# Kernel optimization log

Hardware: AMD Instinct MI355X
Metric: run time of the kernel (lower is better)

The kernel has to match this reference:

```python
import jax, jax.numpy as jnp
import numpy as np

N, E, C, NE, G, T = 20000, 320000, 32, 10, 64, 1000
NB, HID, LAYERS = 8, 64, 2
R_MAX, P_CUT, AVG_NEIGH = 5.0, 6, 16.0
LM = 16  # (max_ell+1)^2 spherical-harmonic components
L_OF_LM = jnp.array([0,1,1,1,2,2,2,2,2,3,3,3,3,3,3,3])


def sph_harm(u):
    # component-normalized real spherical harmonics up to l=3 on unit vectors u [E,3]
    x, y, z = u[:, 0], u[:, 1], u[:, 2]
    s3, s15, s5, s105, s7 = 3**0.5, 15**0.5, 5**0.5, 105**0.5, 7**0.5
    s35_8, s21_8 = (35.0/8.0)**0.5, (21.0/8.0)**0.5
    comps = [jnp.ones_like(x),
             s3*x, s3*y, s3*z,
             s15*x*y, s15*y*z, 0.5*s5*(3*z*z-1.0), s15*x*z, 0.5*s15*(x*x-y*y),
             s35_8*y*(3*x*x-y*y), s105*x*y*z, s21_8*y*(5*z*z-1.0),
             0.5*s7*(5*z*z*z-3*z), s21_8*x*(5*z*z-1.0),
             0.5*s105*z*(x*x-y*y), s35_8*x*(x*x-3*y*y)]
    return jnp.stack(comps, axis=-1)  # [E,16]


def radial_embed(r):
    # Bessel basis with polynomial cutoff (MACE RadialEmbeddingBlock)
    n = jnp.arange(1, NB + 1, dtype=r.dtype)
    rc = jnp.maximum(r, 1e-9)
    bessel = (2.0/R_MAX)**0.5 * jnp.sin(n[None, :]*jnp.pi*rc[:, None]/R_MAX) / rc[:, None]
    xr = r / R_MAX
    p = float(P_CUT)
    f = (1.0 - 0.5*(p+1)*(p+2)*xr**p + p*(p+2)*xr**(p+1) - 0.5*p*(p+1)*xr**(p+2))
    f = f * (xr < 1.0)
    return bessel * f[:, None]  # [E,NB]


def setup_inputs():
    key = jax.random.key(0)
    ks = jax.random.split(key, 16)
    positions = jax.random.normal(ks[0], (N, 3)) * 3.0
    species = jax.random.randint(ks[1], (N,), 0, NE)
    node_attrs = jax.nn.one_hot(species, NE, dtype=jnp.float32)
    edge_index = jax.random.randint(ks[2], (2, E), 0, N)
    shifts = jnp.zeros((E, 3), jnp.float32)
    batch = jnp.sort(jax.random.randint(ks[3], (N,), 0, G))
    t = jax.random.randint(ks[4], (G,), 0, T)
    eps = jax.random.normal(ks[5], (N, NE + 3))
    betas = jnp.linspace(1e-4, 0.02, T)
    alpha_bar = jnp.cumprod(1.0 - betas)
    sc = 0.1
    W_embed = sc * jax.random.normal(ks[6], (NE + 1, C))
    W_r1 = sc * jax.random.normal(ks[7], (LAYERS, NB, HID))
    W_r2 = sc * jax.random.normal(ks[8], (LAYERS, HID, C * 4))
    W_mix = sc * jax.random.normal(ks[9], (LAYERS, 4, C, C))
    W_sc = sc * jax.random.normal(ks[10], (NE, C))
    W_prod = sc * jax.random.normal(ks[11], (LAYERS, 3, C))
    W_ro_s = sc * jax.random.normal(ks[12], (LAYERS, C, NE))
    W_ro_v = sc * jax.random.normal(ks[13], (LAYERS, C))
    return {"positions": positions, "node_attrs": node_attrs, "shifts": shifts,
            "eps": eps, "alpha_bar": alpha_bar, "W_embed": W_embed, "W_r1": W_r1,
            "W_r2": W_r2, "W_mix": W_mix, "W_sc": W_sc, "W_prod": W_prod,
            "W_ro_s": W_ro_s, "W_ro_v": W_ro_v, "edge_index": edge_index,
            "batch": batch, "t": t}


def reference(positions, node_attrs, shifts, eps, alpha_bar, W_embed, W_r1, W_r2,
              W_mix, W_sc, W_prod, W_ro_s, W_ro_v, edge_index, batch, t):
    sender, receiver = edge_index[0], edge_index[1]
    # diffusion: noise positions and attrs (DDPM q(x_t|x_0))
    ab = alpha_bar[t][batch][:, None]                       # [N,1]
    attrs0 = node_attrs / 4.0
    pos_noisy = jnp.sqrt(ab) * positions + jnp.sqrt(1.0 - ab) * eps[:, -3:]
    attrs_noisy = jnp.sqrt(ab) * attrs0 + jnp.sqrt(1.0 - ab) * eps[:, :NE]
    tf = (t.astype(jnp.float32) / T)[batch][:, None]
    h = jnp.concatenate([attrs_noisy, tf], axis=-1) @ W_embed  # [N,C]
    # edge geometry
    vec = pos_noisy[receiver] - pos_noisy[sender] + shifts
    r = jnp.sqrt(jnp.sum(vec * vec, axis=-1) + 1e-12)
    Y = sph_harm(vec / r[:, None])                          # [E,16]
    ef = radial_embed(r)                                    # [E,NB]
    scalar = h
    pred = jnp.zeros((N, NE + 3), h.dtype)
    for layer in range(LAYERS):
        rw = jax.nn.silu(ef @ W_r1[layer]) @ W_r2[layer]    # [E,4C]
        rw = rw.reshape(E, C, 4)[:, :, L_OF_LM]             # [E,C,16]
        msg = rw * scalar[sender][:, :, None] * Y[:, None, :]
        agg = jax.ops.segment_sum(msg, receiver, num_segments=N) / AVG_NEIGH
        Wm = W_mix[layer][L_OF_LM]                          # [16,C,C]
        feats = jnp.einsum('nck,kcd->ndk', agg, Wm)         # per-l channel mix
        s = feats[:, :, 0]
        poly = W_prod[layer, 0] + W_prod[layer, 1] * s + W_prod[layer, 2] * s * s
        feats = feats * poly[:, :, None]                    # correlation-3 product
        if layer == 0:
            feats = feats.at[:, :, 0].add(attrs_noisy @ W_sc)  # element skip
        scalar = feats[:, :, 0]
        pred_s = scalar @ W_ro_s[layer]                     # [N,NE]
        pred_v = jnp.einsum('ncm,c->nm', feats[:, :, 1:4], W_ro_v[layer])  # [N,3]
        pred = pred + jnp.concatenate([pred_s, pred_v], axis=-1)
    err = (pred - eps) ** 2
    loss_pos = jax.ops.segment_sum(err[:, -3:].sum(-1), batch, num_segments=G)
    loss_lab = jax.ops.segment_sum(err[:, :NE].sum(-1), batch, num_segments=G)
    nn = jax.ops.segment_sum(jnp.ones((N,), pred.dtype), batch, num_segments=G)
    loss = 0.5 * (loss_pos + loss_lab) / (jnp.maximum(nn, 1.0) * (3 + NE))
    return loss
```

## Files before the change

kernel.cpp:

```cpp
#include <hip/hip_runtime.h>

typedef unsigned short ushort_t;
typedef unsigned int uint_t;

#define NN 20000
#define EE 320000
#define CC 32
#define NEL 10
#define GG 64
#define TTT 1000
#define NBB 8
#define HIDD 64
#define EPB 256

typedef __attribute__((ext_vector_type(8))) short bf16x8;
typedef __attribute__((ext_vector_type(4))) float f32x4;

__device__ __forceinline__ float bits2f(uint_t b) { union { uint_t u; float f; } v; v.u = b; return v.f; }
__device__ __forceinline__ ushort_t f2b(float f) {
  union { float f; uint_t u; } v; v.f = f;
  uint_t r = (v.u + 0x7fffu + ((v.u >> 16) & 1u)) >> 16;
  return (ushort_t)r;
}
__device__ __forceinline__ uint_t pk(float a, float b) {
  return (uint_t)f2b(a) | ((uint_t)f2b(b) << 16);
}
__device__ __forceinline__ float lo16(uint_t u) { return bits2f(u << 16); }
__device__ __forceinline__ float hi16(uint_t u) { return bits2f(u & 0xffff0000u); }

__global__ __launch_bounds__(256) void k_prep(
    const float* __restrict__ positions, const float* __restrict__ node_attrs,
    const float* __restrict__ eps, const float* __restrict__ alpha_bar,
    const float* __restrict__ W_embed, const float* __restrict__ W_sc,
    const int* __restrict__ batch, const int* __restrict__ tarr,
    float* __restrict__ pos_noisy, float* __restrict__ scalA,
    float* __restrict__ sc_skip, float* __restrict__ pred, int* __restrict__ deg)
{
  int n = blockIdx.x * 256 + threadIdx.x;
  if (n >= NN) return;
  deg[n] = 0;
  int g = batch[n];
  int tn = tarr[g];
  float ab = alpha_bar[tn];
  float sa = sqrtf(ab), sb = sqrtf(fmaxf(1.0f - ab, 0.0f));
#pragma unroll
  for (int j = 0; j < 3; ++j)
    pos_noisy[n * 3 + j] = sa * positions[n * 3 + j] + sb * eps[n * 13 + 10 + j];
  float an[10];
#pragma unroll
  for (int j = 0; j < 10; ++j)
    an[j] = sa * 0.25f * node_attrs[n * 10 + j] + sb * eps[n * 13 + j];
  float tf = (float)tn * (1.0f / (float)TTT);
  for (int d = 0; d < CC; ++d) {
    float h = tf * W_embed[10 * CC + d];
    float sk = 0.0f;
#pragma unroll
    for (int j = 0; j < 10; ++j) {
      h = fmaf(an[j], W_embed[j * CC + d], h);
      sk = fmaf(an[j], W_sc[j * CC + d], sk);
    }
    scalA[n * CC + d] = h;
    sc_skip[n * CC + d] = sk;
  }
#pragma unroll
  for (int j = 0; j < 13; ++j) pred[n * 13 + j] = 0.0f;
}

__global__ __launch_bounds__(256) void k_edge_deg(const int* __restrict__ ei,
    int* __restrict__ deg)
{
  int e = blockIdx.x * 256 + threadIdx.x;
  atomicAdd(&deg[ei[EE + e]], 1);
}

__global__ __launch_bounds__(1024) void k_scan(const int* __restrict__ deg,
    int* __restrict__ offs, int* __restrict__ cursor,
    float* __restrict__ lnum, float* __restrict__ lcnt)
{
  __shared__ int wsums[16];
  __shared__ int woffs[16];
  int tid = threadIdx.x, lane = tid & 63, wv = tid >> 6;
  if (tid < GG) { lnum[tid] = 0.0f; lcnt[tid] = 0.0f; }
  int base = tid * 20;
  int loc[20];
  int s = 0;
#pragma unroll
  for (int j = 0; j < 20; ++j) {
    int idx = base + j;
    int v = (idx < NN) ? deg[idx] : 0;
    loc[j] = s; s += v;
  }
  int inc = s;
  for (int o = 1; o < 64; o <<= 1) {
    int v = __shfl_up(inc, o, 64);
    if (lane >= o) inc += v;
  }
  if (lane == 63) wsums[wv] = inc;
  __syncthreads();
  if (wv == 0 && lane < 16) {
    int v = wsums[lane];
    int i2 = v;
    for (int o = 1; o < 16; o <<= 1) {
      int vv = __shfl_up(i2, o, 16);
      if (lane >= o) i2 += vv;
    }
    woffs[lane] = i2 - v;
  }
  __syncthreads();
  int texcl = woffs[wv] + (inc - s);
#pragma unroll
  for (int j = 0; j < 20; ++j) {
    int idx = base + j;
    if (idx < NN) { int v = texcl + loc[j]; offs[idx] = v; cursor[idx] = v; }
  }
  if (tid == 1023) offs[NN] = EE;
}

__global__ __launch_bounds__(256) void k_edge2(
    const float* __restrict__ pos_noisy, const float* __restrict__ shifts,
    const int* __restrict__ ei, int* __restrict__ cursor,
    ushort_t* __restrict__ Ys, ushort_t* __restrict__ efs, int* __restrict__ snds)
{
  int e = blockIdx.x * 256 + threadIdx.x;
  int snd = ei[e], rcv = ei[EE + e];
  float vx = pos_noisy[rcv * 3 + 0] - pos_noisy[snd * 3 + 0] + shifts[e * 3 + 0];
  float vy = pos_noisy[rcv * 3 + 1] - pos_noisy[snd * 3 + 1] + shifts[e * 3 + 1];
  float vz = pos_noisy[rcv * 3 + 2] - pos_noisy[snd * 3 + 2] + shifts[e * 3 + 2];
  float r2 = vx * vx + vy * vy + vz * vz + 1e-12f;
  float r = sqrtf(r2);
  float inv = 1.0f / r;
  float x = vx * inv, y = vy * inv, z = vz * inv;

  const float s3 = 1.7320508075688772f, s15 = 3.872983346207417f, s5 = 2.23606797749979f;
  const float s105 = 10.246950765959598f, s7 = 2.6457513110645907f;
  const float s35_8 = 2.091650066335189f, s21_8 = 1.6201851746019651f;
  float yv[16];
  yv[0] = 1.0f;
  yv[1] = s3 * x; yv[2] = s3 * y; yv[3] = s3 * z;
  yv[4] = s15 * x * y;
  yv[5] = s15 * y * z;
  yv[6] = 0.5f * s5 * (3.0f * z * z - 1.0f);
  yv[7] = s15 * x * z;
  yv[8] = 0.5f * s15 * (x * x - y * y);
  yv[9] = s35_8 * y * (3.0f * x * x - y * y);
  yv[10] = s105 * x * y * z;
  yv[11] = s21_8 * y * (5.0f * z * z - 1.0f);
  yv[12] = 0.5f * s7 * (5.0f * z * z * z - 3.0f * z);
  yv[13] = s21_8 * x * (5.0f * z * z - 1.0f);
  yv[14] = 0.5f * s105 * z * (x * x - y * y);
  yv[15] = s35_8 * x * (x * x - 3.0f * y * y);

  float rc = fmaxf(r, 1e-9f);
  float pref = 0.6324555320336759f / rc;
  float th = 0.6283185307179586f * rc;
  float s1 = __sinf(th), c1 = __cosf(th);
  float xr = r * 0.2f;
  float fcut = 0.0f;
  if (xr < 1.0f) {
    float x2 = xr * xr, x3 = x2 * xr;
    float x6 = x3 * x3, x7 = x6 * xr, x8 = x7 * xr;
    fcut = 1.0f - 28.0f * x6 + 48.0f * x7 - 21.0f * x8;
  }
  float efv[8];
  float sp = 0.0f, scur = s1, c2 = 2.0f * c1;
#pragma unroll
  for (int b = 0; b < 8; ++b) {
    efv[b] = pref * scur * fcut;
    float nx = c2 * scur - sp;
    sp = scur; scur = nx;
  }

  int slot = atomicAdd(&cursor[rcv], 1);
  snds[slot] = snd;
  uint4* Y4 = (uint4*)Ys;
  Y4[(size_t)slot * 2 + 0] = make_uint4(pk(yv[0], yv[1]), pk(yv[2], yv[3]),
                                        pk(yv[4], yv[5]), pk(yv[6], yv[7]));
  Y4[(size_t)slot * 2 + 1] = make_uint4(pk(yv[8], yv[9]), pk(yv[10], yv[11]),
                                        pk(yv[12], yv[13]), pk(yv[14], yv[15]));
  ((uint4*)efs)[slot] = make_uint4(pk(efv[0], efv[1]), pk(efv[2], efv[3]),
                                   pk(efv[4], efv[5]), pk(efv[6], efv[7]));
}

__global__ __launch_bounds__(256) void k_rw_mfma(
    const ushort_t* __restrict__ efs, const float* __restrict__ W_r1,
    const float* __restrict__ W_r2, const int* __restrict__ snds,
    const float* __restrict__ scal_in, ushort_t* __restrict__ rwc, int layer)
{
  __shared__ __align__(16) ushort_t w2t[128][72];
  __shared__ __align__(16) ushort_t h1[EPB][72];
  int tid = threadIdx.x;
  const float* W1g = W_r1 + layer * NBB * HIDD;
  const float* W2g = W_r2 + layer * HIDD * 128;
  for (int idx = tid; idx < HIDD * 128; idx += 256) {
    int k = idx >> 7, n = idx & 127;
    w2t[n][k] = f2b(W2g[idx]);
  }
  {
    int e = blockIdx.x * EPB + tid;
    uint4 q = ((const uint4*)efs)[e];
    float efr[8] = {lo16(q.x), hi16(q.x), lo16(q.y), hi16(q.y),
                    lo16(q.z), hi16(q.z), lo16(q.w), hi16(q.w)};
    for (int hc = 0; hc < 8; ++hc) {
      float v[8];
#pragma unroll
      for (int hh = 0; hh < 8; ++hh) {
        int h = hc * 8 + hh;
        float t = 0.0f;
#pragma unroll
        for (int b = 0; b < 8; ++b) t = fmaf(efr[b], W1g[b * HIDD + h], t);
        v[hh] = t / (1.0f + __expf(-t));
      }
      *(uint4*)&h1[tid][hc * 8] = make_uint4(pk(v[0], v[1]), pk(v[2], v[3]),
                                             pk(v[4], v[5]), pk(v[6], v[7]));
    }
  }
  __syncthreads();
  int w = tid >> 6, lane = tid & 63;
  int c = lane & 15, quad = lane >> 4;
  bf16x8 bfr[16];
#pragma unroll
  for (int nt = 0; nt < 8; ++nt)
#pragma unroll
    for (int kt = 0; kt < 2; ++kt)
      bfr[nt * 2 + kt] = *(const bf16x8*)&w2t[nt * 16 + c][kt * 32 + quad * 8];
  int mb0 = w * 64;
#pragma unroll
  for (int mt = 0; mt < 4; ++mt) {
    int mbase = mb0 + mt * 16;
    bf16x8 a0 = *(const bf16x8*)&h1[mbase + c][quad * 8];
    bf16x8 a1 = *(const bf16x8*)&h1[mbase + c][32 + quad * 8];
    size_t erow = (size_t)blockIdx.x * EPB + mbase + quad * 4;
    int4 sn = *(const int4*)&snds[erow];
    const float* sb0 = scal_in + (size_t)sn.x * CC;
    const float* sb1 = scal_in + (size_t)sn.y * CC;
    const float* sb2 = scal_in + (size_t)sn.z * CC;
    const float* sb3 = scal_in + (size_t)sn.w * CC;
#pragma unroll
    for (int nt = 0; nt < 8; ++nt) {
      f32x4 acc = {0.0f, 0.0f, 0.0f, 0.0f};
      acc = __builtin_amdgcn_mfma_f32_16x16x32_bf16(a0, bfr[nt * 2 + 0], acc, 0, 0, 0);
      acc = __builtin_amdgcn_mfma_f32_16x16x32_bf16(a1, bfr[nt * 2 + 1], acc, 0, 0, 0);
      int col = nt * 16 + c;
      int cc = col >> 2;
      rwc[(erow + 0) * 128 + col] = f2b(acc[0] * sb0[cc]);
      rwc[(erow + 1) * 128 + col] = f2b(acc[1] * sb1[cc]);
      rwc[(erow + 2) * 128 + col] = f2b(acc[2] * sb2[cc]);
      rwc[(erow + 3) * 128 + col] = f2b(acc[3] * sb3[cc]);
    }
  }
}

__global__ __launch_bounds__(256) void k_layer(
    const ushort_t* __restrict__ Ys, const ushort_t* __restrict__ rwc,
    float* __restrict__ scal_out,
    const int* __restrict__ offs,
    const float* __restrict__ W_mix, const float* __restrict__ W_prod,
    const float* __restrict__ W_ro_s, const float* __restrict__ W_ro_v,
    const float* __restrict__ sc_skip, float* __restrict__ pred, int layer)
{
  __shared__ float lagg[4][CC][16];
  __shared__ float lf[4][CC][4];
  int w = threadIdx.x >> 6, lane = threadIdx.x & 63;
  int n = blockIdx.x * 4 + w;
  int c = lane >> 1;
  int kh = lane & 1;
  int kb = kh * 8;
  int i0 = offs[n], i1 = offs[n + 1];
  float acc0 = 0, acc1 = 0, acc2 = 0, acc3 = 0, acc4 = 0, acc5 = 0, acc6 = 0, acc7 = 0;
  const uint4* Y4 = (const uint4*)Ys;
  const uint2* rw2 = (const uint2*)rwc;
  int s = i0;
  for (; s + 2 <= i1; s += 2) {
    uint4 qa = Y4[(size_t)s * 2 + kh];
    uint2 ra = rw2[(size_t)s * 32 + c];
    uint4 qb = Y4[(size_t)(s + 1) * 2 + kh];
    uint2 rb = rw2[(size_t)(s + 1) * 32 + c];
    {
      float r0 = lo16(ra.x), r1 = hi16(ra.x), r2v = lo16(ra.y), r3 = hi16(ra.y);
      float w0 = kh ? r2v : r0, w13 = kh ? r3 : r1, w47 = kh ? r3 : r2v;
      acc0 = fmaf(w0,  lo16(qa.x), acc0);
      acc1 = fmaf(w13, hi16(qa.x), acc1);
      acc2 = fmaf(w13, lo16(qa.y), acc2);
      acc3 = fmaf(w13, hi16(qa.y), acc3);
      acc4 = fmaf(w47, lo16(qa.z), acc4);
      acc5 = fmaf(w47, hi16(qa.z), acc5);
      acc6 = fmaf(w47, lo16(qa.w), acc6);
      acc7 = fmaf(w47, hi16(qa.w), acc7);
    }
    {
      float r0 = lo16(rb.x), r1 = hi16(rb.x), r2v = lo16(rb.y), r3 = hi16(rb.y);
      float w0 = kh ? r2v : r0, w13 = kh ? r3 : r1, w47 = kh ? r3 : r2v;
      acc0 = fmaf(w0,  lo16(qb.x), acc0);
      acc1 = fmaf(w13, hi16(qb.x), acc1);
      acc2 = fmaf(w13, lo16(qb.y), acc2);
      acc3 = fmaf(w13, hi16(qb.y), acc3);
      acc4 = fmaf(w47, lo16(qb.z), acc4);
      acc5 = fmaf(w47, hi16(qb.z), acc5);
      acc6 = fmaf(w47, lo16(qb.w), acc6);
      acc7 = fmaf(w47, hi16(qb.w), acc7);
    }
  }
  if (s < i1) {
    uint4 q = Y4[(size_t)s * 2 + kh];
    uint2 rp = rw2[(size_t)s * 32 + c];
    float r0 = lo16(rp.x), r1 = hi16(rp.x), r2v = lo16(rp.y), r3 = hi16(rp.y);
    float w0 = kh ? r2v : r0, w13 = kh ? r3 : r1, w47 = kh ? r3 : r2v;
    acc0 = fmaf(w0,  lo16(q.x), acc0);
    acc1 = fmaf(w13, hi16(q.x), acc1);
    acc2 = fmaf(w13, lo16(q.y), acc2);
    acc3 = fmaf(w13, hi16(q.y), acc3);
    acc4 = fmaf(w47, lo16(q.z), acc4);
    acc5 = fmaf(w47, hi16(q.z), acc5);
    acc6 = fmaf(w47, lo16(q.w), acc6);
    acc7 = fmaf(w47, hi16(q.w), acc7);
  }
  const float invavg = 1.0f / 16.0f;
  lagg[w][c][kb + 0] = acc0 * invavg;
  lagg[w][c][kb + 1] = acc1 * invavg;
  lagg[w][c][kb + 2] = acc2 * invavg;
  lagg[w][c][kb + 3] = acc3 * invavg;
  lagg[w][c][kb + 4] = acc4 * invavg;
  lagg[w][c][kb + 5] = acc5 * invavg;
  lagg[w][c][kb + 6] = acc6 * invavg;
  lagg[w][c][kb + 7] = acc7 * invavg;
  __syncthreads();
  int d = c;
  float ft[8] = {0, 0, 0, 0, 0, 0, 0, 0};
  const float* Wm = W_mix + layer * 4096;
  for (int cc2 = 0; cc2 < CC; ++cc2) {
    float m0 = Wm[cc2 * CC + d];
    float m1 = Wm[1024 + cc2 * CC + d];
    float m2 = Wm[2048 + cc2 * CC + d];
    float m3 = Wm[3072 + cc2 * CC + d];
    float u0 = kh ? m2 : m0;
    float u13 = kh ? m3 : m1;
    float u47 = kh ? m3 : m2;
    ft[0] = fmaf(lagg[w][cc2][kb + 0], u0, ft[0]);
    ft[1] = fmaf(lagg[w][cc2][kb + 1], u13, ft[1]);
    ft[2] = fmaf(lagg[w][cc2][kb + 2], u13, ft[2]);
    ft[3] = fmaf(lagg[w][cc2][kb + 3], u13, ft[3]);
    ft[4] = fmaf(lagg[w][cc2][kb + 4], u47, ft[4]);
    ft[5] = fmaf(lagg[w][cc2][kb + 5], u47, ft[5]);
    ft[6] = fmaf(lagg[w][cc2][kb + 6], u47, ft[6]);
    ft[7] = fmaf(lagg[w][cc2][kb + 7], u47, ft[7]);
  }
  float sv = __shfl(ft[0], lane & 62, 64);
  const float* Wp = W_prod + layer * 96;
  float p0 = Wp[d], p1 = Wp[32 + d], p2 = Wp[64 + d];
  float poly = fmaf(fmaf(p2, sv, p1), sv, p0);
#pragma unroll
  for (int j = 0; j < 8; ++j) ft[j] *= poly;
  if (layer == 0 && kh == 0) ft[0] += sc_skip[n * CC + d];
  if (kh == 0) {
    scal_out[n * CC + d] = ft[0];
    lf[w][d][0] = ft[0]; lf[w][d][1] = ft[1]; lf[w][d][2] = ft[2]; lf[w][d][3] = ft[3];
  }
  __syncthreads();
  if (lane < 13) {
    float sum = 0.0f;
    if (lane < 10) {
      const float* Wr = W_ro_s + layer * CC * NEL;
      for (int dd = 0; dd < CC; ++dd) sum = fmaf(lf[w][dd][0], Wr[dd * NEL + lane], sum);
    } else {
      int mm = lane - 10;
      const float* Wv = W_ro_v + layer * CC;
      for (int dd = 0; dd < CC; ++dd) sum = fmaf(lf[w][dd][1 + mm], Wv[dd], sum);
    }
    pred[n * 13 + lane] += sum;
  }
}

__global__ __launch_bounds__(256) void k_loss(const float* __restrict__ pred,
    const float* __restrict__ eps, const int* __restrict__ batch,
    float* __restrict__ lnum, float* __restrict__ lcnt)
{
  __shared__ float psum[GG];
  __shared__ int pcnt[GG];
  int tid = threadIdx.x;
  if (tid < GG) { psum[tid] = 0.0f; pcnt[tid] = 0; }
  __syncthreads();
  int n = blockIdx.x * 256 + tid;
  if (n < NN) {
    int g = batch[n];
    float sum = 0.0f;
#pragma unroll
    for (int j = 0; j < 13; ++j) {
      float dlt = pred[n * 13 + j] - eps[n * 13 + j];
      sum = fmaf(dlt, dlt, sum);
    }
    atomicAdd(&psum[g], sum);
    atomicAdd(&pcnt[g], 1);
  }
  __syncthreads();
  if (tid < GG && pcnt[tid] > 0) {
    atomicAdd(&lnum[tid], psum[tid]);
    atomicAdd(&lcnt[tid], (float)pcnt[tid]);
  }
}

__global__ void k_final(const float* __restrict__ lnum, const float* __restrict__ lcnt,
    float* __restrict__ out)
{
  int g = threadIdx.x;
  if (g < GG) {
    float nn = fmaxf(lcnt[g], 1.0f);
    out[g] = 0.5f * lnum[g] / (nn * 13.0f);
  }
}

extern "C" void kernel_launch(void* const* d_in, const int* in_sizes, int n_in,
                              void* d_out, int out_size, void* d_ws, size_t ws_size,
                              hipStream_t stream) {
  const float* positions  = (const float*)d_in[0];
  const float* node_attrs = (const float*)d_in[1];
  const float* shifts     = (const float*)d_in[2];
  const float* eps        = (const float*)d_in[3];
  const float* alpha_bar  = (const float*)d_in[4];
  const float* W_embed    = (const float*)d_in[5];
  const float* W_r1       = (const float*)d_in[6];
  const float* W_r2       = (const float*)d_in[7];
  const float* W_mix      = (const float*)d_in[8];
  const float* W_sc       = (const float*)d_in[9];
  const float* W_prod     = (const float*)d_in[10];
  const float* W_ro_s     = (const float*)d_in[11];
  const float* W_ro_v     = (const float*)d_in[12];
  const int* edge_index   = (const int*)d_in[13];
  const int* batch        = (const int*)d_in[14];
  const int* tarr         = (const int*)d_in[15];
  float* out = (float*)d_out;

  char* ws = (char*)d_ws;
  size_t off = 0;
  auto alloc = [&](size_t bytes) -> void* {
    void* p = ws + off;
    off = (off + bytes + 255) & ~(size_t)255;
    return p;
  };
  float* pos_noisy = (float*)alloc(NN * 3 * 4);
  float* scalA     = (float*)alloc(NN * CC * 4);
  float* scalB     = (float*)alloc(NN * CC * 4);
  float* sc_skip   = (float*)alloc(NN * CC * 4);
  float* pred      = (float*)alloc(NN * 13 * 4);
  ushort_t* Ys     = (ushort_t*)alloc((size_t)EE * 16 * 2);
  ushort_t* efs    = (ushort_t*)alloc((size_t)EE * 8 * 2);
  int* snds        = (int*)alloc((size_t)EE * 4);
  ushort_t* rwc    = (ushort_t*)alloc((size_t)EE * 128 * 2);
  int* deg         = (int*)alloc(NN * 4);
  int* offs        = (int*)alloc((NN + 1) * 4);
  int* cursor      = (int*)alloc(NN * 4);
  float* lnum      = (float*)alloc(GG * 4);
  float* lcnt      = (float*)alloc(GG * 4);
  (void)ws_size; (void)in_sizes; (void)n_in; (void)out_size;

  const int NB_N = (NN + 255) / 256;
  const int NB_E = EE / 256;

  k_prep<<<NB_N, 256, 0, stream>>>(positions, node_attrs, eps, alpha_bar, W_embed,
                                   W_sc, batch, tarr, pos_noisy, scalA, sc_skip, pred, deg);
  k_edge_deg<<<NB_E, 256, 0, stream>>>(edge_index, deg);
  k_scan<<<1, 1024, 0, stream>>>(deg, offs, cursor, lnum, lcnt);
  k_edge2<<<NB_E, 256, 0, stream>>>(pos_noisy, shifts, edge_index, cursor, Ys, efs, snds);

  for (int layer = 0; layer < 2; ++layer) {
    const float* sin_p = (layer == 0) ? scalA : scalB;
    float* sout_p      = (layer == 0) ? scalB : scalA;
    k_rw_mfma<<<NB_E, 256, 0, stream>>>(efs, W_r1, W_r2, snds, sin_p, rwc, layer);
    k_layer<<<NN / 4, 256, 0, stream>>>(Ys, rwc, sout_p, offs,
                                        W_mix, W_prod, W_ro_s, W_ro_v,
                                        sc_skip, pred, layer);
  }

  k_loss<<<NB_N, 256, 0, stream>>>(pred, eps, batch, lnum, lcnt);
  k_final<<<1, 64, 0, stream>>>(lnum, lcnt, out);
}
```

Baseline: 341.7 us.

## Aggregate edge messages with MFMA over 16-edge tiles using transposed layouts

Replaces the per-node scalar FMA loop over sorted edges with bf16 MFMA over 16-edge tiles. Edges outside the node's range are masked to zero in the Y operand. The radial weights and spherical harmonics are now stored tile-transposed, which needs a new transpose kernel for Y and a new store layout in k_rw_mfma. The layout change also turns scattered 16-bit stores into packed 8-byte stores. The cost is extra work: boundary tiles are loaded and multiplied partly for nothing, 16 l-columns are computed where only 4 are needed, and there is an extra kernel launch.

Measured after the change: 333.1 us. -2.5%, faster.

```diff
diff --git a/kernel.cpp b/kernel.cpp
--- a/kernel.cpp
+++ b/kernel.cpp
@@ -12,6 +12,7 @@
 #define NBB 8
 #define HIDD 64
 #define EPB 256
+#define NTILE (EE / 16)
 
 typedef __attribute__((ext_vector_type(8))) short bf16x8;
 typedef __attribute__((ext_vector_type(4))) float f32x4;
@@ -181,10 +182,27 @@
                                    pk(efv[4], efv[5]), pk(efv[6], efv[7]));
 }
 
+__global__ __launch_bounds__(256) void k_ytr(const ushort_t* __restrict__ Ys,
+    ushort_t* __restrict__ YT)
+{
+  int idx = blockIdx.x * 256 + threadIdx.x;
+  int tile = idx >> 4, k = idx & 15;
+  ushort_t v[16];
+#pragma unroll
+  for (int el = 0; el < 16; ++el)
+    v[el] = Ys[(size_t)(tile * 16 + el) * 16 + k];
+  uint_t u[8];
+#pragma unroll
+  for (int p = 0; p < 8; ++p) u[p] = (uint_t)v[2 * p] | ((uint_t)v[2 * p + 1] << 16);
+  uint4* o = (uint4*)(YT + (size_t)tile * 256 + (size_t)k * 16);
+  o[0] = make_uint4(u[0], u[1], u[2], u[3]);
+  o[1] = make_uint4(u[4], u[5], u[6], u[7]);
+}
+
 __global__ __launch_bounds__(256) void k_rw_mfma(
     const ushort_t* __restrict__ efs, const float* __restrict__ W_r1,
     const float* __restrict__ W_r2, const int* __restrict__ snds,
-    const float* __restrict__ scal_in, ushort_t* __restrict__ rwc, int layer)
+    const float* __restrict__ scal_in, ushort_t* __restrict__ rwT, int layer)
 {
   __shared__ __align__(16) ushort_t w2t[128][72];
   __shared__ __align__(16) ushort_t h1[EPB][72];
@@ -235,6 +253,7 @@
     const float* sb1 = scal_in + (size_t)sn.y * CC;
     const float* sb2 = scal_in + (size_t)sn.z * CC;
     const float* sb3 = scal_in + (size_t)sn.w * CC;
+    int tile = blockIdx.x * 16 + w * 4 + mt;
 #pragma unroll
     for (int nt = 0; nt < 8; ++nt) {
       f32x4 acc = {0.0f, 0.0f, 0.0f, 0.0f};
@@ -242,16 +261,16 @@
       acc = __builtin_amdgcn_mfma_f32_16x16x32_bf16(a1, bfr[nt * 2 + 1], acc, 0, 0, 0);
       int col = nt * 16 + c;
       int cc = col >> 2;
-      rwc[(erow + 0) * 128 + col] = f2b(acc[0] * sb0[cc]);
-      rwc[(erow + 1) * 128 + col] = f2b(acc[1] * sb1[cc]);
-      rwc[(erow + 2) * 128 + col] = f2b(acc[2] * sb2[cc]);
-      rwc[(erow + 3) * 128 + col] = f2b(acc[3] * sb3[cc]);
+      uint2 st;
+      st.x = pk(acc[0] * sb0[cc], acc[1] * sb1[cc]);
+      st.y = pk(acc[2] * sb2[cc], acc[3] * sb3[cc]);
+      *(uint2*)(rwT + (size_t)tile * 2048 + (size_t)col * 16 + quad * 4) = st;
     }
   }
 }
 
 __global__ __launch_bounds__(256) void k_layer(
-    const ushort_t* __restrict__ Ys, const ushort_t* __restrict__ rwc,
+    const ushort_t* __restrict__ YT, const ushort_t* __restrict__ rwT,
     float* __restrict__ scal_out,
     const int* __restrict__ offs,
     const float* __restrict__ W_mix, const float* __restrict__ W_prod,
@@ -262,69 +281,56 @@
   __shared__ float lf[4][CC][4];
   int w = threadIdx.x >> 6, lane = threadIdx.x & 63;
   int n = blockIdx.x * 4 + w;
-  int c = lane >> 1;
+  int c = lane & 15, quad = lane >> 4;
+  int i0 = offs[n], i1 = offs[n + 1];
+  int t0 = i0 >> 4, t1 = (i1 + 15) >> 4;
+  int tsel = quad >> 1, half8 = quad & 1;
+  f32x4 acc[8];
+#pragma unroll
+  for (int mt = 0; mt < 8; ++mt) acc[mt] = (f32x4){0.0f, 0.0f, 0.0f, 0.0f};
+
+  for (int t = t0; t < t1; t += 2) {
+    int ta = t + tsel;
+    bf16x8 a[8];
+    bf16x8 b;
+    bool tv = (ta * 16 < i1) && (ta * 16 + 16 > i0);
+    if (tv) {
+      const bf16x8* ap = (const bf16x8*)rwT + (size_t)ta * 256 + c * 2 + half8;
+#pragma unroll
+      for (int mt = 0; mt < 8; ++mt) a[mt] = ap[mt * 32];
+      b = ((const bf16x8*)YT)[(size_t)ta * 32 + c * 2 + half8];
+      if (ta * 16 < i0 || ta * 16 + 16 > i1) {
+        int sbase = ta * 16 + half8 * 8;
+#pragma unroll
+        for (int j = 0; j < 8; ++j) {
+          int s = sbase + j;
+          if (s < i0 || s >= i1) b[j] = 0;
+        }
+      }
+    } else {
+#pragma unroll
+      for (int mt = 0; mt < 8; ++mt) a[mt] = (bf16x8){0, 0, 0, 0, 0, 0, 0, 0};
+      b = (bf16x8){0, 0, 0, 0, 0, 0, 0, 0};
+    }
+#pragma unroll
+    for (int mt = 0; mt < 8; ++mt)
+      acc[mt] = __builtin_amdgcn_mfma_f32_16x16x32_bf16(a[mt], b, acc[mt], 0, 0, 0);
+  }
+
+  int lc = (c >= 1) + (c >= 4) + (c >= 9);
+  const float inva = 1.0f / 16.0f;
+#pragma unroll
+  for (int mt = 0; mt < 8; ++mt) {
+    float v = (lc == 0) ? acc[mt][0] : (lc == 1) ? acc[mt][1]
+            : (lc == 2) ? acc[mt][2] : acc[mt][3];
+    lagg[w][mt * 4 + quad][c] = v * inva;
+  }
+  __syncthreads();
+
+  int c2 = lane >> 1;
   int kh = lane & 1;
   int kb = kh * 8;
-  int i0 = offs[n], i1 = offs[n + 1];
-  float acc0 = 0, acc1 = 0, acc2 = 0, acc3 = 0, acc4 = 0, acc5 = 0, acc6 = 0, acc7 = 0;
-  const uint4* Y4 = (const uint4*)Ys;
-  const uint2* rw2 = (const uint2*)rwc;
-  int s = i0;
-  for (; s + 2 <= i1; s += 2) {
-    uint4 qa = Y4[(size_t)s * 2 + kh];
-    uint2 ra = rw2[(size_t)s * 32 + c];
-    uint4 qb = Y4[(size_t)(s + 1) * 2 + kh];
-    uint2 rb = rw2[(size_t)(s + 1) * 32 + c];
-    {
-      float r0 = lo16(ra.x), r1 = hi16(ra.x), r2v = lo16(ra.y), r3 = hi16(ra.y);
-      float w0 = kh ? r2v : r0, w13 = kh ? r3 : r1, w47 = kh ? r3 : r2v;
-      acc0 = fmaf(w0,  lo16(qa.x), acc0);
-      acc1 = fmaf(w13, hi16(qa.x), acc1);
-      acc2 = fmaf(w13, lo16(qa.y), acc2);
-      acc3 = fmaf(w13, hi16(qa.y), acc3);
-      acc4 = fmaf(w47, lo16(qa.z), acc4);
-      acc5 = fmaf(w47, hi16(qa.z), acc5);
-      acc6 = fmaf(w47, lo16(qa.w), acc6);
-      acc7 = fmaf(w47, hi16(qa.w), acc7);
-    }
-    {
-      float r0 = lo16(rb.x), r1 = hi16(rb.x), r2v = lo16(rb.y), r3 = hi16(rb.y);
-      float w0 = kh ? r2v : r0, w13 = kh ? r3 : r1, w47 = kh ? r3 : r2v;
-      acc0 = fmaf(w0,  lo16(qb.x), acc0);
-      acc1 = fmaf(w13, hi16(qb.x), acc1);
-      acc2 = fmaf(w13, lo16(qb.y), acc2);
-      acc3 = fmaf(w13, hi16(qb.y), acc3);
-      acc4 = fmaf(w47, lo16(qb.z), acc4);
-      acc5 = fmaf(w47, hi16(qb.z), acc5);
-      acc6 = fmaf(w47, lo16(qb.w), acc6);
-      acc7 = fmaf(w47, hi16(qb.w), acc7);
-    }
-  }
-  if (s < i1) {
-    uint4 q = Y4[(size_t)s * 2 + kh];
-    uint2 rp = rw2[(size_t)s * 32 + c];
-    float r0 = lo16(rp.x), r1 = hi16(rp.x), r2v = lo16(rp.y), r3 = hi16(rp.y);
-    float w0 = kh ? r2v : r0, w13 = kh ? r3 : r1, w47 = kh ? r3 : r2v;
-    acc0 = fmaf(w0,  lo16(q.x), acc0);
-    acc1 = fmaf(w13, hi16(q.x), acc1);
-    acc2 = fmaf(w13, lo16(q.y), acc2);
-    acc3 = fmaf(w13, hi16(q.y), acc3);
-    acc4 = fmaf(w47, lo16(q.z), acc4);
-    acc5 = fmaf(w47, hi16(q.z), acc5);
-    acc6 = fmaf(w47, lo16(q.w), acc6);
-    acc7 = fmaf(w47, hi16(q.w), acc7);
-  }
-  const float invavg = 1.0f / 16.0f;
-  lagg[w][c][kb + 0] = acc0 * invavg;
-  lagg[w][c][kb + 1] = acc1 * invavg;
-  lagg[w][c][kb + 2] = acc2 * invavg;
-  lagg[w][c][kb + 3] = acc3 * invavg;
-  lagg[w][c][kb + 4] = acc4 * invavg;
-  lagg[w][c][kb + 5] = acc5 * invavg;
-  lagg[w][c][kb + 6] = acc6 * invavg;
-  lagg[w][c][kb + 7] = acc7 * invavg;
-  __syncthreads();
-  int d = c;
+  int d = c2;
   float ft[8] = {0, 0, 0, 0, 0, 0, 0, 0};
   const float* Wm = W_mix + layer * 4096;
   for (int cc2 = 0; cc2 < CC; ++cc2) {
@@ -442,9 +448,10 @@
   float* sc_skip   = (float*)alloc(NN * CC * 4);
   float* pred      = (float*)alloc(NN * 13 * 4);
   ushort_t* Ys     = (ushort_t*)alloc((size_t)EE * 16 * 2);
+  ushort_t* YT     = (ushort_t*)alloc((size_t)NTILE * 256 * 2);
   ushort_t* efs    = (ushort_t*)alloc((size_t)EE * 8 * 2);
   int* snds        = (int*)alloc((size_t)EE * 4);
-  ushort_t* rwc    = (ushort_t*)alloc((size_t)EE * 128 * 2);
+  ushort_t* rwT    = (ushort_t*)alloc((size_t)NTILE * 2048 * 2);
   int* deg         = (int*)alloc(NN * 4);
   int* offs        = (int*)alloc((NN + 1) * 4);
   int* cursor      = (int*)alloc(NN * 4);
@@ -460,12 +467,13 @@
   k_edge_deg<<<NB_E, 256, 0, stream>>>(edge_index, deg);
   k_scan<<<1, 1024, 0, stream>>>(deg, offs, cursor, lnum, lcnt);
   k_edge2<<<NB_E, 256, 0, stream>>>(pos_noisy, shifts, edge_index, cursor, Ys, efs, snds);
+  k_ytr<<<NB_E, 256, 0, stream>>>(Ys, YT);
 
   for (int layer = 0; layer < 2; ++layer) {
     const float* sin_p = (layer == 0) ? scalA : scalB;
     float* sout_p      = (layer == 0) ? scalB : scalA;
-    k_rw_mfma<<<NB_E, 256, 0, stream>>>(efs, W_r1, W_r2, snds, sin_p, rwc, layer);
-    k_layer<<<NN / 4, 256, 0, stream>>>(Ys, rwc, sout_p, offs,
+    k_rw_mfma<<<NB_E, 256, 0, stream>>>(efs, W_r1, W_r2, snds, sin_p, rwT, layer);
+    k_layer<<<NN / 4, 256, 0, stream>>>(YT, rwT, sout_p, offs,
                                         W_mix, W_prod, W_ro_s, W_ro_v,
                                         sc_skip, pred, layer);
   }
```
